# Kernel tuning notes

Hardware: AMD Instinct MI355X
Metric: run time of the kernel (lower is better)

## Reference

```python
import math
import jax, jax.numpy as jnp
import numpy as np

INITIAL_TEMP = 0.2
FINAL_TEMP = 0.05
TOTAL_ITERS = 300000
B, M, D = 4096, 4, 512


def get_temperature(iteration):
    if iteration >= TOTAL_ITERS:
        return FINAL_TEMP
    progress = iteration / TOTAL_ITERS
    return FINAL_TEMP + 0.5 * (INITIAL_TEMP - FINAL_TEMP) * (1 + math.cos(math.pi * progress))


def _l2_normalize(x, axis=-1, eps=1e-12):
    # matches F.normalize(p=2): x / max(||x||, eps)
    n = jnp.sqrt(jnp.sum(x * x, axis=axis, keepdims=True))
    return x / jnp.maximum(n, eps)


def setup_inputs() -> dict:
    key = jax.random.key(0)
    k1, k2 = jax.random.split(key)
    return {
        "original_emb": jax.random.normal(k1, (B, D), dtype=jnp.float32),
        "masked_embs": jax.random.normal(k2, (M, B, D), dtype=jnp.float32),
        "iteration": 0,
    }


def reference(original_emb, masked_embs, iteration):
    temperature = get_temperature(iteration)
    orig_n = _l2_normalize(original_emb, axis=1)          # [B, D]
    masked_n = _l2_normalize(masked_embs, axis=2)         # [M, B, D]
    # all_embeddings = cat([orig] + masked), shape [N, D], N = (M+1)*B
    all_emb = jnp.concatenate([orig_n[None], masked_n], axis=0).reshape((M + 1) * B, D)
    # Loss only uses the first B rows of the NxN sim matrix -> compute [B, N] block.
    sim = jnp.matmul(orig_n, all_emb.T) / temperature     # [B, N]
    rows = jnp.arange(B)
    # self-mask: for rows i < B the diagonal entry is column i
    is_diag = rows[:, None] == jnp.arange((M + 1) * B)[None, :]
    sim = jnp.where(is_diag, -1e9, sim)
    exp_sim = jnp.exp(sim)                                # [B, N]
    denom = exp_sim.sum(axis=1) - jnp.exp(sim[rows, rows])  # exp(-1e9) == 0
    # positives: columns (m+1)*B + i for m in 0..M-1
    e = exp_sim.reshape(B, M + 1, B)
    pos = e[rows, :, rows][:, 1:].sum(axis=1)             # [B]
    loss = -jnp.log(pos / (denom + 1e-8))
    return loss.mean()
```

## Files before the change

kernel.cpp:

```cpp
#include <hip/hip_runtime.h>
#include <math.h>


#define B_ROWS 4096
#define M_MASK 4
#define D_DIM  512
#define N_COLS ((M_MASK + 1) * B_ROWS)
#define GK     D_DIM
#define NT     (GK / 32)

typedef _Float16 f16x8 __attribute__((ext_vector_type(8)));
typedef float    f32x4 __attribute__((ext_vector_type(4)));

__device__ __forceinline__ float inv_temp(const int* __restrict__ itp) {
    int it = *itp;
    double T;
    if (it >= 300000) {
        T = 0.05;
    } else {
        double p = (double)it / 300000.0;
        T = 0.05 + 0.5 * (0.2 - 0.05) * (1.0 + cos(3.14159265358979323846 * p));
    }
    return (float)(1.0 / T);
}

__global__ __launch_bounds__(256) void prep_kernel(
        const float* __restrict__ orig, const float* __restrict__ masked,
        _Float16* __restrict__ E) {
    int gw = blockIdx.x * 4 + (threadIdx.x >> 6);
    int l  = threadIdx.x & 63;
    if (gw >= N_COLS) return;
    const float* row = (gw < B_ROWS) ? orig + (size_t)gw * D_DIM
                                     : masked + (size_t)(gw - B_ROWS) * D_DIM;
    float4 a = *(const float4*)(row + l * 8);
    float4 b = *(const float4*)(row + l * 8 + 4);
    float s = a.x*a.x + a.y*a.y + a.z*a.z + a.w*a.w
            + b.x*b.x + b.y*b.y + b.z*b.z + b.w*b.w;
    #pragma unroll
    for (int off = 1; off < 64; off <<= 1) s += __shfl_xor(s, off, 64);
    float inv = 1.0f / fmaxf(sqrtf(s), 1e-12f);

    f16x8 h;
    h[0] = (_Float16)(a.x*inv); h[1] = (_Float16)(a.y*inv);
    h[2] = (_Float16)(a.z*inv); h[3] = (_Float16)(a.w*inv);
    h[4] = (_Float16)(b.x*inv); h[5] = (_Float16)(b.y*inv);
    h[6] = (_Float16)(b.z*inv); h[7] = (_Float16)(b.w*inv);
    *(f16x8*)(E + (size_t)gw * GK + l * 8) = h;
}

__global__ __launch_bounds__(256, 3) void gemm_kernel(
        const _Float16* __restrict__ E, const int* __restrict__ itp,
        float* __restrict__ denom, float* __restrict__ pos) {
    __shared__ _Float16 LDS[3 * 8192];

    const int tid = threadIdx.x;
    const int l   = tid & 63;
    const int wid = tid >> 6;
    const int wr  = wid >> 1;
    const int wc  = wid & 1;

    const int rowTile = blockIdx.x & 31;
    const int colTile = blockIdx.x >> 5;
    const int rowBase = rowTile * 128;
    const int colBase = colTile * 128;

    const _Float16* Ag = E + (size_t)rowBase * GK;
    const _Float16* Bg = E + (size_t)colBase * GK;

    auto STAGE = [&](int t) {
        _Float16* base = LDS + (t % 3) * 8192;
        const int kb = t * 32;
        #pragma unroll
        for (int i = 0; i < 2; ++i) {
            const int rc = wid * 32 + i * 16;
            const int r  = rc + (l >> 2);
            const size_t go = (size_t)r * GK + kb + (l & 3) * 8;
            __builtin_amdgcn_global_load_lds(
                (const __attribute__((address_space(1))) void*)(Ag + go),
                (__attribute__((address_space(3))) void*)(base + rc * 32), 16, 0, 0);
            __builtin_amdgcn_global_load_lds(
                (const __attribute__((address_space(1))) void*)(Bg + go),
                (__attribute__((address_space(3))) void*)(base + 4096 + rc * 32), 16, 0, 0);
        }
    };

    f16x8 af[4], bf[4];
    auto FRAGS = [&](int t) {
        const _Float16* base = LDS + (t % 3) * 8192;
        #pragma unroll
        for (int m = 0; m < 4; ++m)
            af[m] = *(const f16x8*)(base + (wr * 64 + m * 16 + (l & 15)) * 32 + (l >> 4) * 8);
        #pragma unroll
        for (int n = 0; n < 4; ++n)
            bf[n] = *(const f16x8*)(base + 4096 + (wc * 64 + n * 16 + (l & 15)) * 32 + (l >> 4) * 8);
    };

    f32x4 acc[4][4];
    #pragma unroll
    for (int m = 0; m < 4; ++m)
        #pragma unroll
        for (int n = 0; n < 4; ++n)
            #pragma unroll
            for (int j = 0; j < 4; ++j) acc[m][n][j] = 0.f;

    auto MM = [&]() {
        __builtin_amdgcn_s_setprio(1);
        #pragma unroll
        for (int m = 0; m < 4; ++m)
            #pragma unroll
            for (int n = 0; n < 4; ++n)
                acc[m][n] = __builtin_amdgcn_mfma_f32_16x16x32_f16(af[m], bf[n], acc[m][n], 0, 0, 0);
        __builtin_amdgcn_s_setprio(0);
    };

#define BAR()  __builtin_amdgcn_s_barrier()
#define LGKM0() { asm volatile("s_waitcnt lgkmcnt(0)" ::: "memory"); \
                  __builtin_amdgcn_sched_barrier(0); }
#define VM(n)  asm volatile("s_waitcnt vmcnt(" #n ")" ::: "memory")

    STAGE(0); STAGE(1);
    VM(4);
    BAR();

    for (int t = 0; t < NT - 2; ++t) {
        STAGE(t + 2);
        FRAGS(t);
        VM(4);
        BAR();
        LGKM0();
        MM();
        BAR();
    }
    FRAGS(NT - 2);
    VM(0);
    BAR();
    LGKM0();
    MM();
    BAR();
    FRAGS(NT - 1);
    LGKM0();
    MM();

    const float scale = inv_temp(itp) * 1.44269504088896340736f;
    float dsum[16];
    #pragma unroll
    for (int i = 0; i < 16; ++i) dsum[i] = 0.f;

    #pragma unroll
    for (int m = 0; m < 4; ++m) {
        #pragma unroll
        for (int n = 0; n < 4; ++n) {
            const int col = colBase + wc * 64 + n * 16 + (l & 15);
            #pragma unroll
            for (int r = 0; r < 4; ++r) {
                const int row = rowBase + wr * 64 + m * 16 + (l >> 4) * 4 + r;
                float e = exp2f(acc[m][n][r] * scale);
                if (col == row) e = 0.f;
                dsum[m * 4 + r] += e;
                const int d = col - row;
                if (d > 0 && (d & (B_ROWS - 1)) == 0) atomicAdd(&pos[row], e);
            }
        }
    }
    #pragma unroll
    for (int i = 0; i < 16; ++i) {
        #pragma unroll
        for (int off = 1; off < 16; off <<= 1)
            dsum[i] += __shfl_xor(dsum[i], off, 64);
    }
    if ((l & 15) == 0) {
        #pragma unroll
        for (int i = 0; i < 16; ++i) {
            const int row = rowBase + wr * 64 + (i >> 2) * 16 + (l >> 4) * 4 + (i & 3);
            atomicAdd(&denom[row], dsum[i]);
        }
    }
#undef BAR
#undef LGKM0
#undef VM
}

__global__ __launch_bounds__(256) void loss_kernel(
        const float* __restrict__ denom, const float* __restrict__ pos,
        float* __restrict__ out) {
    __shared__ double buf[256];
    double s = 0.0;
    for (int i = threadIdx.x; i < B_ROWS; i += 256) {
        float p = pos[i];
        float d = denom[i] + 1e-8f;
        s += (double)(-logf(p / d));
    }
    buf[threadIdx.x] = s;
    __syncthreads();
    for (int off = 128; off >= 1; off >>= 1) {
        if (threadIdx.x < off) buf[threadIdx.x] += buf[threadIdx.x + off];
        __syncthreads();
    }
    if (threadIdx.x == 0) out[0] = (float)(buf[0] / (double)B_ROWS);
}

extern "C" void kernel_launch(void* const* d_in, const int* in_sizes, int n_in,
                              void* d_out, int out_size, void* d_ws, size_t ws_size,
                              hipStream_t stream) {
    const float* orig   = (const float*)d_in[0];
    const float* masked = (const float*)d_in[1];
    const int*   itp    = (const int*)d_in[2];

    _Float16* E   = (_Float16*)d_ws;
    float* denom  = (float*)(E + (size_t)N_COLS * GK);
    float* pos    = denom + B_ROWS;
    float* out    = (float*)d_out;

    hipMemsetAsync(denom, 0, 2 * B_ROWS * sizeof(float), stream);

    prep_kernel<<<N_COLS / 4, 256, 0, stream>>>(orig, masked, E);

    gemm_kernel<<<(B_ROWS / 128) * (N_COLS / 128), 256, 0, stream>>>(E, itp, denom, pos);

    loss_kernel<<<1, 256, 0, stream>>>(denom, pos, out);
}
```

Before: 209.3 us.

## Fuse memset and loss reduction into kernels, swizzle LDS fragment layout

Zeroing of the denom/pos accumulators moves into an extra block of the prep kernel. The final loss reduction runs in the last-finishing gemm block, chosen with an atomic ticket, which removes the memset and the separate loss launch. The LDS k-chunk placement is also XOR-swizzled on both the global->LDS load and the fragment read, to reduce bank conflicts. This adds a threadfence/atomic ticket per block and atomic reads in the tail.

```diff
diff --git a/kernel.cpp b/kernel.cpp
--- a/kernel.cpp
+++ b/kernel.cpp
@@ -26,10 +26,17 @@
 
 __global__ __launch_bounds__(256) void prep_kernel(
         const float* __restrict__ orig, const float* __restrict__ masked,
-        _Float16* __restrict__ E) {
+        _Float16* __restrict__ E, float* __restrict__ zbuf, int* __restrict__ ticket) {
+    if (blockIdx.x == N_COLS / 4) {
+        float4 z = {0.f, 0.f, 0.f, 0.f};
+        #pragma unroll
+        for (int i = 0; i < 8; ++i)
+            *(float4*)(zbuf + threadIdx.x * 4 + i * 1024) = z;
+        if (threadIdx.x == 0) *ticket = 0;
+        return;
+    }
     int gw = blockIdx.x * 4 + (threadIdx.x >> 6);
     int l  = threadIdx.x & 63;
-    if (gw >= N_COLS) return;
     const float* row = (gw < B_ROWS) ? orig + (size_t)gw * D_DIM
                                      : masked + (size_t)(gw - B_ROWS) * D_DIM;
     float4 a = *(const float4*)(row + l * 8);
@@ -50,7 +57,8 @@
 
 __global__ __launch_bounds__(256, 3) void gemm_kernel(
         const _Float16* __restrict__ E, const int* __restrict__ itp,
-        float* __restrict__ denom, float* __restrict__ pos) {
+        float* __restrict__ denom, float* __restrict__ pos,
+        int* __restrict__ ticket, float* __restrict__ out) {
     __shared__ _Float16 LDS[3 * 8192];
 
     const int tid = threadIdx.x;
@@ -67,6 +75,7 @@
     const _Float16* Ag = E + (size_t)rowBase * GK;
     const _Float16* Bg = E + (size_t)colBase * GK;
 
+    const int ksrc = (((l & 3) ^ ((l >> 3) & 3)) * 8);
     auto STAGE = [&](int t) {
         _Float16* base = LDS + (t % 3) * 8192;
         const int kb = t * 32;
@@ -74,7 +83,7 @@
         for (int i = 0; i < 2; ++i) {
             const int rc = wid * 32 + i * 16;
             const int r  = rc + (l >> 2);
-            const size_t go = (size_t)r * GK + kb + (l & 3) * 8;
+            const size_t go = (size_t)r * GK + kb + ksrc;
             __builtin_amdgcn_global_load_lds(
                 (const __attribute__((address_space(1))) void*)(Ag + go),
                 (__attribute__((address_space(3))) void*)(base + rc * 32), 16, 0, 0);
@@ -84,15 +93,16 @@
         }
     };
 
+    const int koff = (((l >> 4) ^ ((l >> 1) & 3)) * 8);
     f16x8 af[4], bf[4];
     auto FRAGS = [&](int t) {
         const _Float16* base = LDS + (t % 3) * 8192;
         #pragma unroll
         for (int m = 0; m < 4; ++m)
-            af[m] = *(const f16x8*)(base + (wr * 64 + m * 16 + (l & 15)) * 32 + (l >> 4) * 8);
+            af[m] = *(const f16x8*)(base + (wr * 64 + m * 16 + (l & 15)) * 32 + koff);
         #pragma unroll
         for (int n = 0; n < 4; ++n)
-            bf[n] = *(const f16x8*)(base + 4096 + (wc * 64 + n * 16 + (l & 15)) * 32 + (l >> 4) * 8);
+            bf[n] = *(const f16x8*)(base + 4096 + (wc * 64 + n * 16 + (l & 15)) * 32 + koff);
     };
 
     f32x4 acc[4][4];
@@ -178,25 +188,29 @@
 #undef BAR
 #undef LGKM0
 #undef VM
-}
-
-__global__ __launch_bounds__(256) void loss_kernel(
-        const float* __restrict__ denom, const float* __restrict__ pos,
-        float* __restrict__ out) {
-    __shared__ double buf[256];
-    double s = 0.0;
-    for (int i = threadIdx.x; i < B_ROWS; i += 256) {
-        float p = pos[i];
-        float d = denom[i] + 1e-8f;
-        s += (double)(-logf(p / d));
-    }
-    buf[threadIdx.x] = s;
+
+    __shared__ int lastFlag;
+    if (tid == 0) {
+        __threadfence();
+        lastFlag = (atomicAdd(ticket, 1) == (int)gridDim.x - 1) ? 1 : 0;
+    }
     __syncthreads();
-    for (int off = 128; off >= 1; off >>= 1) {
-        if (threadIdx.x < off) buf[threadIdx.x] += buf[threadIdx.x + off];
+    if (lastFlag) {
+        double s = 0.0;
+        for (int i = tid; i < B_ROWS; i += 256) {
+            float p = atomicAdd(&pos[i], 0.0f);
+            float d = atomicAdd(&denom[i], 0.0f);
+            s += (double)(-logf(p / (d + 1e-8f)));
+        }
+        double* buf = (double*)LDS;
+        buf[tid] = s;
         __syncthreads();
-    }
-    if (threadIdx.x == 0) out[0] = (float)(buf[0] / (double)B_ROWS);
+        for (int off = 128; off >= 1; off >>= 1) {
+            if (tid < off) buf[tid] += buf[tid + off];
+            __syncthreads();
+        }
+        if (tid == 0) out[0] = (float)(buf[0] / (double)B_ROWS);
+    }
 }
 
 extern "C" void kernel_launch(void* const* d_in, const int* in_sizes, int n_in,
@@ -209,13 +223,10 @@
     _Float16* E   = (_Float16*)d_ws;
     float* denom  = (float*)(E + (size_t)N_COLS * GK);
     float* pos    = denom + B_ROWS;
+    int*   ticket = (int*)(pos + B_ROWS);
     float* out    = (float*)d_out;
 
-    hipMemsetAsync(denom, 0, 2 * B_ROWS * sizeof(float), stream);
-
-    prep_kernel<<<N_COLS / 4, 256, 0, stream>>>(orig, masked, E);
-
-    gemm_kernel<<<(B_ROWS / 128) * (N_COLS / 128), 256, 0, stream>>>(E, itp, denom, pos);
-
-    loss_kernel<<<1, 256, 0, stream>>>(denom, pos, out);
-}
+    prep_kernel<<<N_COLS / 4 + 1, 256, 0, stream>>>(orig, masked, E, denom, ticket);
+
+    gemm_kernel<<<(B_ROWS / 128) * (N_COLS / 128), 256, 0, stream>>>(E, itp, denom, pos, ticket, out);
+}
```

New measurement: 296.1 us. 1.41x slower.
